# Kernel tuning notes

Measured on AMD Instinct MI355X. Metric: run time of the kernel, lower is better.

Reference implementation:

```python
import jax, jax.numpy as jnp
import numpy as np

N, E = 20000, 320000
H1, C1 = 8, 128   # gat1 heads/out
H2, C2 = 1, 128   # gat2 heads/out
D_IN = 768
NEG_SLOPE = 0.2
BN_EPS = 1e-5


def setup_inputs() -> dict:
    key = jax.random.key(0)
    ks = jax.random.split(key, 16)
    def rn(k, shape, fan):
        return jax.random.normal(k, shape, dtype=jnp.float32) / np.sqrt(fan)
    x = jax.random.normal(ks[0], (N, D_IN), dtype=jnp.float32)
    edge_index = jax.random.randint(ks[1], (2, E), 0, N, dtype=jnp.int64)
    return {
        "x": x,
        "edge_index": edge_index,
        "W1": rn(ks[2], (D_IN, H1 * C1), D_IN),
        "att_src1": rn(ks[3], (H1, C1), C1),
        "att_dst1": rn(ks[4], (H1, C1), C1),
        "b1": jnp.zeros((H1 * C1,), jnp.float32),
        "W2": rn(ks[5], (H1 * C1, H2 * C2), H1 * C1),
        "att_src2": rn(ks[6], (H2, C2), C2),
        "att_dst2": rn(ks[7], (H2, C2), C2),
        "b2": jnp.zeros((C2,), jnp.float32),
        "g1": jnp.ones((H1 * C1,), jnp.float32),
        "be1": jnp.zeros((H1 * C1,), jnp.float32),
        "g2": jnp.ones((C2,), jnp.float32),
        "be2": jnp.zeros((C2,), jnp.float32),
        "Wc1": rn(ks[8], (C2, 64), C2),
        "bc1": jnp.zeros((64,), jnp.float32),
        "Wc2": rn(ks[9], (64, 2), 64),
        "bc2": jnp.zeros((2,), jnp.float32),
    }


def gat_conv(x, src, dst, W, att_src, att_dst, bias, heads, ch, concat):
    n = x.shape[0]
    h = (x @ W).reshape(n, heads, ch)                      # [N,H,C]
    a_s = jnp.sum(h * att_src[None], axis=-1)              # [N,H]
    a_d = jnp.sum(h * att_dst[None], axis=-1)
    e = a_s[src] + a_d[dst]                                # [Et,H]
    e = jax.nn.leaky_relu(e, NEG_SLOPE)
    # segment softmax over incoming edges of each dst node
    m = jax.ops.segment_max(e, dst, num_segments=n)
    ex = jnp.exp(e - m[dst])
    z = jax.ops.segment_sum(ex, dst, num_segments=n)
    alpha = ex / z[dst]                                    # [Et,H]
    msg = alpha[:, :, None] * h[src]                       # [Et,H,C]
    out = jax.ops.segment_sum(msg, dst, num_segments=n)    # [N,H,C]
    if concat:
        out = out.reshape(n, heads * ch)
    else:
        out = out.mean(axis=1)
    return out + bias


def batch_norm(x, gamma, beta):
    mu = x.mean(axis=0)
    var = x.var(axis=0)
    return (x - mu) * jax.lax.rsqrt(var + BN_EPS) * gamma + beta


def reference(x, edge_index, W1, att_src1, att_dst1, b1, W2, att_src2, att_dst2, b2,
              g1, be1, g2, be2, Wc1, bc1, Wc2, bc2):
    n = x.shape[0]
    loop = jnp.arange(n, dtype=edge_index.dtype)
    src = jnp.concatenate([edge_index[0], loop])  # PyG add_self_loops default
    dst = jnp.concatenate([edge_index[1], loop])
    h = gat_conv(x, src, dst, W1, att_src1, att_dst1, b1, H1, C1, True)
    h = jax.nn.elu(batch_norm(h, g1, be1))
    h = gat_conv(h, src, dst, W2, att_src2, att_dst2, b2, H2, C2, False)
    h = jax.nn.elu(batch_norm(h, g2, be2))
    h = jax.nn.relu(h @ Wc1 + bc1)
    return h @ Wc2 + bc2
```

## Files before the change

kernel.cpp:

```cpp
#include <hip/hip_runtime.h>
#include <hip/hip_bf16.h>
#include <math.h>

#define N_NODES 20000
#define N_EDGES 320000
#define DIN 768
#define F1 1024
#define H1 8
#define C1 128
#define F2 128
#define NEG_SLOPE 0.2f
#define BN_EPS 1e-5f
#define RESCALE_THR 8.0f

typedef __attribute__((ext_vector_type(8))) __bf16 bf16x8;
typedef __attribute__((ext_vector_type(4))) float f32x4;

__device__ __forceinline__ float leaky(float x) { return x > 0.f ? x : NEG_SLOPE * x; }

__device__ __forceinline__ unsigned short f2bu(float x) {
  __hip_bfloat16 b = __float2bfloat16(x);
  return *(unsigned short*)&b;
}
__device__ __forceinline__ float b2f(unsigned short u) {
  return __uint_as_float(((unsigned)u) << 16);
}
__device__ __forceinline__ unsigned pack2(float lo, float hi) {
  return (unsigned)f2bu(lo) | ((unsigned)f2bu(hi) << 16);
}

__device__ __forceinline__ void async_copy16(void* lds, const void* g) {
  __builtin_amdgcn_global_load_lds(
      (const __attribute__((address_space(1))) unsigned int*)g,
      (__attribute__((address_space(3))) unsigned int*)lds, 16, 0, 0);
}

__global__ void repack_hist_kernel(const int* raw, int* ei32, int* deg) {
  int is64 = (raw[1] == 0 && raw[3] == 0 && raw[5] == 0 && raw[7] == 0) ? 1 : 0;
  int e = blockIdx.x * blockDim.x + threadIdx.x;
  if (e < 2 * N_EDGES) {
    int v = is64 ? raw[2 * e] : raw[e];
    ei32[e] = v;
    if (e >= N_EDGES) atomicAdd(&deg[v], 1);
  }
}

#define NPT 20
__global__ __launch_bounds__(1024) void scan_kernel(const int* __restrict__ deg,
                                                    int* __restrict__ off,
                                                    int* __restrict__ cursor) {
  __shared__ int wsum[16];
  int tid = threadIdx.x;
  int lane = tid & 63, wv = tid >> 6;
  int base = tid * NPT;
  int loc[NPT];
  int run = 0;
#pragma unroll
  for (int k = 0; k < NPT; ++k) {
    int i = base + k;
    int v = (i < N_NODES) ? deg[i] : 0;
    loc[k] = run;
    run += v;
  }
  int incl = run;
  for (int sh = 1; sh < 64; sh <<= 1) {
    int t = __shfl_up(incl, sh, 64);
    if (lane >= sh) incl += t;
  }
  if (lane == 63) wsum[wv] = incl;
  __syncthreads();
  if (wv == 0 && lane < 16) {
    int v = wsum[lane];
    for (int sh = 1; sh < 16; sh <<= 1) {
      int t = __shfl_up(v, sh, 16);
      if (lane >= sh) v += t;
    }
    wsum[lane] = v;
  }
  __syncthreads();
  int wbase = (wv > 0) ? wsum[wv - 1] : 0;
  int tbase = wbase + incl - run;
#pragma unroll
  for (int k = 0; k < NPT; ++k) {
    int i = base + k;
    if (i < N_NODES) {
      int o = tbase + loc[k];
      off[i] = o;
      cursor[i] = o;
    }
  }
  if (tid == 1023) off[N_NODES] = wbase + incl;
}

__global__ void scatter_kernel(const int* ei, int* cursor, int* elist) {
  int e = blockIdx.x * blockDim.x + threadIdx.x;
  if (e < N_EDGES) {
    int dst = ei[N_EDGES + e];
    int p = atomicAdd(&cursor[dst], 1);
    elist[p] = ei[e];
  }
}

__global__ void f2b_kernel(const float* __restrict__ in, unsigned short* __restrict__ out,
                           size_t n4) {
  size_t i = (size_t)blockIdx.x * blockDim.x + threadIdx.x;
  size_t stride = (size_t)gridDim.x * blockDim.x;
  for (; i < n4; i += stride) {
    float4 v = ((const float4*)in)[i];
    ushort4 u;
    u.x = f2bu(v.x); u.y = f2bu(v.y); u.z = f2bu(v.z); u.w = f2bu(v.w);
    ((ushort4*)out)[i] = u;
  }
}

__global__ void transpose_b_kernel(const float* __restrict__ W, unsigned short* __restrict__ WT,
                                   int K, int N) {
  __shared__ float t[32][33];
  int k0 = blockIdx.y * 32, n0 = blockIdx.x * 32;
  int tx = threadIdx.x & 31, ty = threadIdx.x >> 5;
  for (int i = 0; i < 32; i += 8)
    t[ty + i][tx] = W[(size_t)(k0 + ty + i) * N + n0 + tx];
  __syncthreads();
  for (int i = 0; i < 32; i += 8)
    WT[(size_t)(n0 + ty + i) * K + k0 + tx] = f2bu(t[tx][ty + i]);
}

#define GBM 128
#define GBN 128
#define GBK 64
template <int H, int SWZ>
__global__ __launch_bounds__(256) void mfma_gemm_att_kernel(
    const unsigned short* __restrict__ A,
    const unsigned short* __restrict__ BT,
    unsigned short* __restrict__ C,
    const float* __restrict__ att_src,
    const float* __restrict__ att_dst,
    float* __restrict__ as_out,
    float* __restrict__ ad_out,
    int M, int N, int K) {
  __shared__ __hip_bfloat16 As[GBM][GBK];
  __shared__ __hip_bfloat16 Bs[GBN][GBK];
  __shared__ float sred[128][2];
  __shared__ float dred[128][2];
  int bx, by;
  if (SWZ) {
    int bid = blockIdx.x;
    int pl = bid & 7, c = (bid >> 3) & 7, ph = bid >> 6;
    int p = ph * 8 + pl;
    if (p * GBM >= M) return;
    by = p; bx = c;
  } else {
    bx = blockIdx.x; by = blockIdx.y;
  }
  int tid = threadIdx.x;
  int lane = tid & 63, wid = tid >> 6;
  int wr = wid >> 1, wc = wid & 1;
  int row0 = by * GBM, col0 = bx * GBN;
  int head = bx;
  int l16 = lane & 15, l4 = lane >> 4;
  f32x4 acc[4][4] = {};
  for (int k0 = 0; k0 < K; k0 += GBK) {
#pragma unroll
    for (int j = 0; j < 4; ++j) {
      int c = j * 256 + tid;
      int r = c >> 3, kk = (c & 7) << 3;
      int ga = row0 + r; if (ga >= M) ga = M - 1;
      async_copy16(&As[r][kk], A + (size_t)ga * K + k0 + kk);
      async_copy16(&Bs[r][kk], BT + (size_t)(col0 + r) * K + k0 + kk);
    }
    __syncthreads();
#pragma unroll
    for (int ks = 0; ks < 2; ++ks) {
      bf16x8 af[4], bfr[4];
#pragma unroll
      for (int i = 0; i < 4; ++i)
        af[i] = *(const bf16x8*)&As[wr * 64 + i * 16 + l16][ks * 32 + l4 * 8];
#pragma unroll
      for (int j = 0; j < 4; ++j)
        bfr[j] = *(const bf16x8*)&Bs[wc * 64 + j * 16 + l16][ks * 32 + l4 * 8];
#pragma unroll
      for (int i = 0; i < 4; ++i)
#pragma unroll
        for (int j = 0; j < 4; ++j)
          acc[i][j] = __builtin_amdgcn_mfma_f32_16x16x32_bf16(af[i], bfr[j], acc[i][j], 0, 0, 0);
    }
    __syncthreads();
  }
#pragma unroll
  for (int i = 0; i < 4; ++i) {
#pragma unroll
    for (int j = 0; j < 4; ++j) {
#pragma unroll
      for (int r = 0; r < 4; ++r) {
        int row = row0 + wr * 64 + i * 16 + l4 * 4 + r;
        int col = col0 + wc * 64 + j * 16 + l16;
        if (row < M) C[(size_t)row * N + col] = f2bu(acc[i][j][r]);
      }
    }
  }
  float avs[4], avd[4];
#pragma unroll
  for (int j = 0; j < 4; ++j) {
    int col = col0 + wc * 64 + j * 16 + l16;
    avs[j] = att_src[col];
    avd[j] = att_dst[col];
  }
#pragma unroll
  for (int i = 0; i < 4; ++i) {
#pragma unroll
    for (int r = 0; r < 4; ++r) {
      float ps = 0.f, pd = 0.f;
#pragma unroll
      for (int j = 0; j < 4; ++j) { ps += acc[i][j][r] * avs[j]; pd += acc[i][j][r] * avd[j]; }
#pragma unroll
      for (int mk = 1; mk < 16; mk <<= 1) {
        ps += __shfl_xor(ps, mk, 64);
        pd += __shfl_xor(pd, mk, 64);
      }
      if (l16 == 0) {
        int lr = wr * 64 + i * 16 + l4 * 4 + r;
        sred[lr][wc] = ps;
        dred[lr][wc] = pd;
      }
    }
  }
  __syncthreads();
  if (tid < 128) {
    int row = row0 + tid;
    if (row < M) {
      as_out[(size_t)row * H + head] = sred[tid][0] + sred[tid][1];
      ad_out[(size_t)row * H + head] = dred[tid][0] + dred[tid][1];
    }
  }
}

__global__ __launch_bounds__(64) void alpha1_kernel(const float* __restrict__ as1,
                                                    const float* __restrict__ ad1,
                                                    const int* __restrict__ off,
                                                    const int* __restrict__ elist,
                                                    float* __restrict__ wexpT,
                                                    float* __restrict__ zinv,
                                                    float* __restrict__ wself) {
  int node = blockIdx.x;
  int lane = threadIdx.x;
  int s = off[node], e = off[node + 1];
#pragma unroll
  for (int h = 0; h < H1; ++h) {
    float ad = ad1[node * H1 + h];
    float selfl = leaky(as1[node * H1 + h] + ad);
    float m = selfl;
    for (int i = s + lane; i < e; i += 64) {
      float el = leaky(as1[elist[i] * H1 + h] + ad);
      m = fmaxf(m, el);
    }
    for (int sh = 32; sh >= 1; sh >>= 1) m = fmaxf(m, __shfl_xor(m, sh, 64));
    float z = 0.f;
    for (int i = s + lane; i < e; i += 64) {
      float el = leaky(as1[elist[i] * H1 + h] + ad);
      float w = __expf(el - m);
      wexpT[(size_t)h * N_EDGES + i] = w;
      z += w;
    }
    for (int sh = 32; sh >= 1; sh >>= 1) z += __shfl_xor(z, sh, 64);
    float ws = __expf(selfl - m);
    if (lane == 0) {
      zinv[node * H1 + h] = 1.f / (z + ws);
      wself[node * H1 + h] = ws;
    }
  }
}

#define GW_LOAD(i, rv, wv)                                                     \
  if ((i) < e) {                                                               \
    wv = wp[(i)];                                                              \
    rv = *(const unsigned*)(h1 + (size_t)elist[(i)] * F1 + cb);                \
  }
#define GW_CONS(u, wv)                                                         \
  {                                                                            \
    a0 += wv * __uint_as_float(u << 16);                                       \
    a1 += wv * __uint_as_float(u & 0xffff0000u);                               \
  }

__global__ __launch_bounds__(64) void gatherw1_kernel(const unsigned short* __restrict__ h1,
                                                      const float* __restrict__ wexpT,
                                                      const float* __restrict__ zinv,
                                                      const float* __restrict__ wself,
                                                      const int* __restrict__ off,
                                                      const int* __restrict__ elist,
                                                      const float* __restrict__ b1,
                                                      unsigned short* __restrict__ out1) {
  int head = blockIdx.x;
  int node = blockIdx.y;
  int tid = threadIdx.x;
  int cb = head * C1 + tid * 2;
  int s = off[node], e = off[node + 1];
  const float* wp = wexpT + (size_t)head * N_EDGES;
  float a0, a1;
  {
    float ws = wself[node * H1 + head];
    unsigned u = *(const unsigned*)(h1 + (size_t)node * F1 + cb);
    a0 = ws * __uint_as_float(u << 16);
    a1 = ws * __uint_as_float(u & 0xffff0000u);
  }
  unsigned ra0 = 0, ra1 = 0, ra2 = 0, ra3 = 0;
  float wa0 = 0.f, wa1 = 0.f, wa2 = 0.f, wa3 = 0.f;
  GW_LOAD(s + 0, ra0, wa0)
  GW_LOAD(s + 1, ra1, wa1)
  GW_LOAD(s + 2, ra2, wa2)
  GW_LOAD(s + 3, ra3, wa3)
  for (int base = s; base < e; base += 4) {
    unsigned rb0 = 0, rb1 = 0, rb2 = 0, rb3 = 0;
    float wb0 = 0.f, wb1 = 0.f, wb2 = 0.f, wb3 = 0.f;
    int nb = base + 4;
    GW_LOAD(nb + 0, rb0, wb0)
    GW_LOAD(nb + 1, rb1, wb1)
    GW_LOAD(nb + 2, rb2, wb2)
    GW_LOAD(nb + 3, rb3, wb3)
    GW_CONS(ra0, wa0)
    GW_CONS(ra1, wa1)
    GW_CONS(ra2, wa2)
    GW_CONS(ra3, wa3)
    ra0 = rb0; ra1 = rb1; ra2 = rb2; ra3 = rb3;
    wa0 = wb0; wa1 = wb1; wa2 = wb2; wa3 = wb3;
  }
  float inv = zinv[node * H1 + head];
  float2 bv = *(const float2*)(b1 + cb);
  unsigned o = pack2(a0 * inv + bv.x, a1 * inv + bv.y);
  *(unsigned*)(out1 + (size_t)node * F1 + cb) = o;
}

__global__ void bnstats_bf16_kernel(const unsigned short* __restrict__ x,
                                    float* __restrict__ sums,
                                    int nrows, int F, int rowsPerBlock) {
  int tid = threadIdx.x;
  int c = tid * 4;
  int r0 = blockIdx.x * rowsPerBlock;
  int rend = min(r0 + rowsPerBlock, nrows);
  float s0 = 0.f, s1 = 0.f, s2 = 0.f, s3 = 0.f;
  float q0 = 0.f, q1 = 0.f, q2 = 0.f, q3 = 0.f;
  for (int r = r0; r < rend; ++r) {
    ushort4 u = *(const ushort4*)(x + (size_t)r * F + c);
    float v0 = b2f(u.x), v1 = b2f(u.y), v2 = b2f(u.z), v3 = b2f(u.w);
    s0 += v0; s1 += v1; s2 += v2; s3 += v3;
    q0 += v0 * v0; q1 += v1 * v1; q2 += v2 * v2; q3 += v3 * v3;
  }
  atomicAdd(&sums[c + 0], s0); atomicAdd(&sums[c + 1], s1);
  atomicAdd(&sums[c + 2], s2); atomicAdd(&sums[c + 3], s3);
  atomicAdd(&sums[F + c + 0], q0); atomicAdd(&sums[F + c + 1], q1);
  atomicAdd(&sums[F + c + 2], q2); atomicAdd(&sums[F + c + 3], q3);
}

template <int CPT>
__global__ void bnstats_kernel(const float* __restrict__ x, float* __restrict__ sums,
                               int nrows, int F, int rowsPerBlock) {
  int tid = threadIdx.x;
  int r0 = blockIdx.x * rowsPerBlock;
  int rend = min(r0 + rowsPerBlock, nrows);
  float s[CPT], q[CPT];
#pragma unroll
  for (int k = 0; k < CPT; ++k) { s[k] = 0.f; q[k] = 0.f; }
  for (int r = r0; r < rend; ++r) {
    const float* row = x + (size_t)r * F;
#pragma unroll
    for (int k = 0; k < CPT; ++k) {
      float v = row[tid + k * blockDim.x];
      s[k] += v; q[k] += v * v;
    }
  }
#pragma unroll
  for (int k = 0; k < CPT; ++k) {
    atomicAdd(&sums[tid + k * blockDim.x], s[k]);
    atomicAdd(&sums[F + tid + k * blockDim.x], q[k]);
  }
}

__global__ void bnfinal_kernel(const float* __restrict__ sums, const float* __restrict__ g,
                               const float* __restrict__ be, float* __restrict__ ss, int F) {
  int c = blockIdx.x * blockDim.x + threadIdx.x;
  if (c < F) {
    float mu = sums[c] * (1.f / N_NODES);
    float var = sums[F + c] * (1.f / N_NODES) - mu * mu;
    float sc = g[c] * rsqrtf(var + BN_EPS);
    ss[c] = sc;
    ss[F + c] = be[c] - mu * sc;
  }
}

__global__ void bnapply_bf16_kernel(unsigned short* __restrict__ x, const float* __restrict__ ss,
                                    int F, size_t total4) {
  size_t i = (size_t)blockIdx.x * blockDim.x + threadIdx.x;
  size_t stride = (size_t)gridDim.x * blockDim.x;
  for (; i < total4; i += stride) {
    int c = (int)((i * 4) & (size_t)(F - 1));
    ushort4 u = ((ushort4*)x)[i];
    float v0 = b2f(u.x) * ss[c + 0] + ss[F + c + 0];
    float v1 = b2f(u.y) * ss[c + 1] + ss[F + c + 1];
    float v2 = b2f(u.z) * ss[c + 2] + ss[F + c + 2];
    float v3 = b2f(u.w) * ss[c + 3] + ss[F + c + 3];
    v0 = v0 > 0.f ? v0 : expm1f(v0);
    v1 = v1 > 0.f ? v1 : expm1f(v1);
    v2 = v2 > 0.f ? v2 : expm1f(v2);
    v3 = v3 > 0.f ? v3 : expm1f(v3);
    u.x = f2bu(v0); u.y = f2bu(v1); u.z = f2bu(v2); u.w = f2bu(v3);
    ((ushort4*)x)[i] = u;
  }
}

#define G2_LOAD(i, rv, ev)                                                     \
  if ((i) < e) {                                                               \
    int ssrc = elist[(i)];                                                     \
    ev = leaky(as2[ssrc] + ad);                                                \
    rv = *(const unsigned*)(h2 + (size_t)ssrc * F2 + tid * 2);                 \
  }
#define G2_CONSUME(u, el)                                                      \
  {                                                                            \
    float w;                                                                   \
    if (el > m + RESCALE_THR) {                                                \
      float rr = __expf(m - el);                                               \
      z *= rr; a0 *= rr; a1 *= rr;                                             \
      m = el; w = 1.f;                                                         \
    } else {                                                                   \
      w = __expf(el - m);                                                      \
    }                                                                          \
    z += w;                                                                    \
    a0 += w * __uint_as_float(u << 16);                                        \
    a1 += w * __uint_as_float(u & 0xffff0000u);                                \
  }

__global__ __launch_bounds__(64) void gather2_kernel(const unsigned short* __restrict__ h2,
                                                     const float* __restrict__ as2,
                                                     const float* __restrict__ ad2,
                                                     const int* __restrict__ off,
                                                     const int* __restrict__ elist,
                                                     const float* __restrict__ b2,
                                                     float* __restrict__ out2) {
  int node = blockIdx.x;
  int tid = threadIdx.x;
  const float ad = ad2[node];
  int s = off[node], e = off[node + 1];
  float m = leaky(as2[node] + ad);
  float z = 1.f;
  float a0, a1;
  {
    unsigned u = *(const unsigned*)(h2 + (size_t)node * F2 + tid * 2);
    a0 = __uint_as_float(u << 16); a1 = __uint_as_float(u & 0xffff0000u);
  }
  unsigned ra0 = 0, ra1 = 0, ra2 = 0, ra3 = 0;
  float ea0 = 0.f, ea1 = 0.f, ea2 = 0.f, ea3 = 0.f;
  G2_LOAD(s + 0, ra0, ea0)
  G2_LOAD(s + 1, ra1, ea1)
  G2_LOAD(s + 2, ra2, ea2)
  G2_LOAD(s + 3, ra3, ea3)
  for (int base = s; base < e; base += 4) {
    unsigned rb0 = 0, rb1 = 0, rb2 = 0, rb3 = 0;
    float eb0 = 0.f, eb1 = 0.f, eb2 = 0.f, eb3 = 0.f;
    int nb = base + 4;
    G2_LOAD(nb + 0, rb0, eb0)
    G2_LOAD(nb + 1, rb1, eb1)
    G2_LOAD(nb + 2, rb2, eb2)
    G2_LOAD(nb + 3, rb3, eb3)
    G2_CONSUME(ra0, ea0)
    if (base + 1 < e) G2_CONSUME(ra1, ea1)
    if (base + 2 < e) G2_CONSUME(ra2, ea2)
    if (base + 3 < e) G2_CONSUME(ra3, ea3)
    ra0 = rb0; ra1 = rb1; ra2 = rb2; ra3 = rb3;
    ea0 = eb0; ea1 = eb1; ea2 = eb2; ea3 = eb3;
  }
  float inv = 1.f / z;
  float2 o = make_float2(a0 * inv + b2[tid * 2 + 0], a1 * inv + b2[tid * 2 + 1]);
  *(float2*)(out2 + (size_t)node * F2 + tid * 2) = o;
}

__global__ __launch_bounds__(64) void cls_kernel(const float* __restrict__ h,
                                                 const float* __restrict__ ss2,
                                                 const float* __restrict__ Wc1,
                                                 const float* __restrict__ bc1,
                                                 const float* __restrict__ Wc2,
                                                 const float* __restrict__ bc2,
                                                 float* __restrict__ out) {
  __shared__ float hl[128];
  int node = blockIdx.x;
  int tid = threadIdx.x;
  {
    float v = h[(size_t)node * F2 + tid] * ss2[tid] + ss2[F2 + tid];
    v = v > 0.f ? v : expm1f(v);
    hl[tid] = v;
    float v2 = h[(size_t)node * F2 + 64 + tid] * ss2[64 + tid] + ss2[F2 + 64 + tid];
    v2 = v2 > 0.f ? v2 : expm1f(v2);
    hl[tid + 64] = v2;
  }
  __syncthreads();
  float acc = bc1[tid];
#pragma unroll
  for (int k = 0; k < 128; ++k) acc += hl[k] * Wc1[k * 64 + tid];
  acc = fmaxf(acc, 0.f);
  float2 w = *(const float2*)(Wc2 + tid * 2);
  float o0 = acc * w.x, o1 = acc * w.y;
  for (int sh = 32; sh >= 1; sh >>= 1) {
    o0 += __shfl_down(o0, sh, 64);
    o1 += __shfl_down(o1, sh, 64);
  }
  if (tid == 0) {
    out[node * 2 + 0] = o0 + bc2[0];
    out[node * 2 + 1] = o1 + bc2[1];
  }
}

extern "C" void kernel_launch(void* const* d_in, const int* in_sizes, int n_in,
                              void* d_out, int out_size, void* d_ws, size_t ws_size,
                              hipStream_t stream) {
  const float* x        = (const float*)d_in[0];
  const int*   ei_raw   = (const int*)d_in[1];
  const float* W1       = (const float*)d_in[2];
  const float* att_src1 = (const float*)d_in[3];
  const float* att_dst1 = (const float*)d_in[4];
  const float* b1       = (const float*)d_in[5];
  const float* W2       = (const float*)d_in[6];
  const float* att_src2 = (const float*)d_in[7];
  const float* att_dst2 = (const float*)d_in[8];
  const float* b2       = (const float*)d_in[9];
  const float* g1       = (const float*)d_in[10];
  const float* be1      = (const float*)d_in[11];
  const float* g2       = (const float*)d_in[12];
  const float* be2      = (const float*)d_in[13];
  const float* Wc1      = (const float*)d_in[14];
  const float* bc1      = (const float*)d_in[15];
  const float* Wc2      = (const float*)d_in[16];
  const float* bc2      = (const float*)d_in[17];
  float* out = (float*)d_out;

  char* ws = (char*)d_ws;
  size_t o = 0;
  unsigned short* h1b   = (unsigned short*)(ws + o); o += (size_t)N_NODES * F1 * 2;
  unsigned short* out1b = (unsigned short*)(ws + o); o += (size_t)N_NODES * F1 * 2;
  unsigned short* xb    = (unsigned short*)(ws + o); o += (size_t)N_NODES * DIN * 2;
  unsigned short* h2b   = (unsigned short*)(ws + o); o += (size_t)N_NODES * F2 * 2;
  float* out2  = (float*)(ws + o); o += (size_t)N_NODES * F2 * 4;
  float* as1   = (float*)(ws + o); o += (size_t)N_NODES * H1 * 4;
  float* ad1   = (float*)(ws + o); o += (size_t)N_NODES * H1 * 4;
  float* as2   = (float*)(ws + o); o += (size_t)N_NODES * 4;
  float* ad2   = (float*)(ws + o); o += (size_t)N_NODES * 4;
  float* wexpT = (float*)(ws + o); o += (size_t)H1 * N_EDGES * 4;
  float* zinv  = (float*)(ws + o); o += (size_t)N_NODES * H1 * 4;
  float* wself = (float*)(ws + o); o += (size_t)N_NODES * H1 * 4;
  char*  zbase = ws + o;
  float* bnsum1 = (float*)(ws + o); o += F1 * 2 * 4;
  float* bnsum2 = (float*)(ws + o); o += F2 * 2 * 4;
  int*   deg    = (int*)(ws + o); o += (size_t)N_NODES * 4;
  size_t zbytes = (size_t)((ws + o) - zbase);
  int*   offv   = (int*)(ws + o); o += (size_t)(N_NODES + 4) * 4;
  int*   cursor = (int*)(ws + o); o += (size_t)N_NODES * 4;
  int*   elist  = (int*)(ws + o); o += (size_t)N_EDGES * 4;
  float* ss1    = (float*)(ws + o); o += F1 * 2 * 4;
  float* ss2    = (float*)(ws + o); o += F2 * 2 * 4;
  int*   ei32   = (int*)(ws + o); o += (size_t)2 * N_EDGES * 4;
  unsigned short* W1T = (unsigned short*)(ws + o); o += (size_t)F1 * DIN * 2;
  unsigned short* W2T = (unsigned short*)(ws + o); o += (size_t)F2 * F1 * 2;
  (void)ws_size; (void)in_sizes; (void)n_in; (void)out_size;

  hipMemsetAsync((void*)zbase, 0, zbytes, stream);

  f2b_kernel<<<2048, 256, 0, stream>>>(x, xb, (size_t)N_NODES * DIN / 4);
  {
    dim3 g1d(F1 / 32, DIN / 32);
    transpose_b_kernel<<<g1d, 256, 0, stream>>>(W1, W1T, DIN, F1);
    dim3 g2d(F2 / 32, F1 / 32);
    transpose_b_kernel<<<g2d, 256, 0, stream>>>(W2, W2T, F1, F2);
  }

  repack_hist_kernel<<<(2 * N_EDGES + 255) / 256, 256, 0, stream>>>(ei_raw, ei32, deg);
  scan_kernel<<<1, 1024, 0, stream>>>(deg, offv, cursor);
  scatter_kernel<<<(N_EDGES + 255) / 256, 256, 0, stream>>>(ei32, cursor, elist);

  {
    int panels = (N_NODES + GBM - 1) / GBM;
    int grid1 = ((panels + 7) / 8) * 64;
    mfma_gemm_att_kernel<H1, 1><<<grid1, 256, 0, stream>>>(
        xb, W1T, h1b, att_src1, att_dst1, as1, ad1, N_NODES, F1, DIN);
  }
  alpha1_kernel<<<N_NODES, 64, 0, stream>>>(as1, ad1, offv, elist, wexpT, zinv, wself);
  gatherw1_kernel<<<dim3(H1, N_NODES), 64, 0, stream>>>(
      h1b, wexpT, zinv, wself, offv, elist, b1, out1b);
  {
    int rows = 79;
    int grid = (N_NODES + rows - 1) / rows;
    bnstats_bf16_kernel<<<grid, 256, 0, stream>>>(out1b, bnsum1, N_NODES, F1, rows);
  }
  bnfinal_kernel<<<(F1 + 255) / 256, 256, 0, stream>>>(bnsum1, g1, be1, ss1, F1);
  bnapply_bf16_kernel<<<2048, 256, 0, stream>>>(out1b, ss1, F1, (size_t)N_NODES * F1 / 4);

  {
    dim3 grid(F2 / GBN, (N_NODES + GBM - 1) / GBM);
    mfma_gemm_att_kernel<1, 0><<<grid, 256, 0, stream>>>(
        out1b, W2T, h2b, att_src2, att_dst2, as2, ad2, N_NODES, F2, F1);
  }
  gather2_kernel<<<N_NODES, 64, 0, stream>>>(h2b, as2, ad2, offv, elist, b2, out2);
  {
    int rows = 79;
    int grid = (N_NODES + rows - 1) / rows;
    bnstats_kernel<1><<<grid, 128, 0, stream>>>(out2, bnsum2, N_NODES, F2, rows);
  }
  bnfinal_kernel<<<1, F2, 0, stream>>>(bnsum2, g2, be2, ss2, F2);

  cls_kernel<<<N_NODES, 64, 0, stream>>>(out2, ss2, Wc1, bc1, Wc2, bc2, out);
}
```

Before: 461.7 us.

## Pack source index with edge weight and deepen gather prefetch pipeline

alpha1 now handles all 8 heads in one pass per edge, loading each source's 8 attention scores as two float4s instead of re-walking the edge list once per head. It writes (src, weight) pairs per head, so the gather kernel no longer does a dependent elist lookup before fetching h1 rows. The gather loop now prefetches edge pairs two stages ahead, which shortens the chain of dependent loads. In exchange the edge-weight buffer doubles in size, so alpha1 writes more bytes and the gather reads more, and register use rises.

```diff
diff --git a/kernel.cpp b/kernel.cpp
--- a/kernel.cpp
+++ b/kernel.cpp
@@ -238,55 +238,74 @@
                                                     const float* __restrict__ ad1,
                                                     const int* __restrict__ off,
                                                     const int* __restrict__ elist,
-                                                    float* __restrict__ wexpT,
+                                                    uint2* __restrict__ ewT,
                                                     float* __restrict__ zinv,
                                                     float* __restrict__ wself) {
   int node = blockIdx.x;
   int lane = threadIdx.x;
   int s = off[node], e = off[node + 1];
-#pragma unroll
-  for (int h = 0; h < H1; ++h) {
-    float ad = ad1[node * H1 + h];
-    float selfl = leaky(as1[node * H1 + h] + ad);
-    float m = selfl;
-    for (int i = s + lane; i < e; i += 64) {
-      float el = leaky(as1[elist[i] * H1 + h] + ad);
-      m = fmaxf(m, el);
-    }
-    for (int sh = 32; sh >= 1; sh >>= 1) m = fmaxf(m, __shfl_xor(m, sh, 64));
-    float z = 0.f;
-    for (int i = s + lane; i < e; i += 64) {
-      float el = leaky(as1[elist[i] * H1 + h] + ad);
-      float w = __expf(el - m);
-      wexpT[(size_t)h * N_EDGES + i] = w;
-      z += w;
-    }
-    for (int sh = 32; sh >= 1; sh >>= 1) z += __shfl_xor(z, sh, 64);
-    float ws = __expf(selfl - m);
-    if (lane == 0) {
-      zinv[node * H1 + h] = 1.f / (z + ws);
+  float4 adlo = *(const float4*)(ad1 + node * H1);
+  float4 adhi = *(const float4*)(ad1 + node * H1 + 4);
+  float ad[8] = {adlo.x, adlo.y, adlo.z, adlo.w, adhi.x, adhi.y, adhi.z, adhi.w};
+  float4 aslo = *(const float4*)(as1 + node * H1);
+  float4 ashi = *(const float4*)(as1 + node * H1 + 4);
+  float sl[8] = {aslo.x, aslo.y, aslo.z, aslo.w, ashi.x, ashi.y, ashi.z, ashi.w};
+  float m[8];
+#pragma unroll
+  for (int h = 0; h < 8; ++h) { sl[h] = leaky(sl[h] + ad[h]); m[h] = sl[h]; }
+  for (int i = s + lane; i < e; i += 64) {
+    int src = elist[i];
+    float4 lo = *(const float4*)(as1 + (size_t)src * H1);
+    float4 hi = *(const float4*)(as1 + (size_t)src * H1 + 4);
+    float v[8] = {lo.x, lo.y, lo.z, lo.w, hi.x, hi.y, hi.z, hi.w};
+#pragma unroll
+    for (int h = 0; h < 8; ++h) m[h] = fmaxf(m[h], leaky(v[h] + ad[h]));
+  }
+#pragma unroll
+  for (int h = 0; h < 8; ++h)
+    for (int sh = 32; sh >= 1; sh >>= 1) m[h] = fmaxf(m[h], __shfl_xor(m[h], sh, 64));
+  float z[8] = {0.f, 0.f, 0.f, 0.f, 0.f, 0.f, 0.f, 0.f};
+  for (int i = s + lane; i < e; i += 64) {
+    int src = elist[i];
+    float4 lo = *(const float4*)(as1 + (size_t)src * H1);
+    float4 hi = *(const float4*)(as1 + (size_t)src * H1 + 4);
+    float v[8] = {lo.x, lo.y, lo.z, lo.w, hi.x, hi.y, hi.z, hi.w};
+#pragma unroll
+    for (int h = 0; h < 8; ++h) {
+      float w = __expf(leaky(v[h] + ad[h]) - m[h]);
+      z[h] += w;
+      ewT[(size_t)h * N_EDGES + i] = make_uint2((unsigned)src, __float_as_uint(w));
+    }
+  }
+#pragma unroll
+  for (int h = 0; h < 8; ++h)
+    for (int sh = 32; sh >= 1; sh >>= 1) z[h] += __shfl_xor(z[h], sh, 64);
+  if (lane == 0) {
+#pragma unroll
+    for (int h = 0; h < 8; ++h) {
+      float ws = __expf(sl[h] - m[h]);
+      zinv[node * H1 + h] = 1.f / (z[h] + ws);
       wself[node * H1 + h] = ws;
     }
   }
 }
 
-#define GW_LOAD(i, rv, wv)                                                     \
-  if ((i) < e) {                                                               \
-    wv = wp[(i)];                                                              \
-    rv = *(const unsigned*)(h1 + (size_t)elist[(i)] * F1 + cb);                \
-  }
-#define GW_CONS(u, wv)                                                         \
-  {                                                                            \
-    a0 += wv * __uint_as_float(u << 16);                                       \
-    a1 += wv * __uint_as_float(u & 0xffff0000u);                               \
+#define EW_LOAD(i, ev)                                                          \
+  if ((i) < e) ev = ewp[(i)];
+#define H1_LOAD(i, ev, rv)                                                      \
+  if ((i) < e) rv = *(const unsigned*)(h1 + (size_t)ev.x * F1 + cb);
+#define GW_CONS(u, ev)                                                          \
+  {                                                                             \
+    float wv = __uint_as_float(ev.y);                                           \
+    a0 += wv * __uint_as_float(u << 16);                                        \
+    a1 += wv * __uint_as_float(u & 0xffff0000u);                                \
   }
 
 __global__ __launch_bounds__(64) void gatherw1_kernel(const unsigned short* __restrict__ h1,
-                                                      const float* __restrict__ wexpT,
+                                                      const uint2* __restrict__ ewT,
                                                       const float* __restrict__ zinv,
                                                       const float* __restrict__ wself,
                                                       const int* __restrict__ off,
-                                                      const int* __restrict__ elist,
                                                       const float* __restrict__ b1,
                                                       unsigned short* __restrict__ out1) {
   int head = blockIdx.x;
@@ -294,7 +313,7 @@
   int tid = threadIdx.x;
   int cb = head * C1 + tid * 2;
   int s = off[node], e = off[node + 1];
-  const float* wp = wexpT + (size_t)head * N_EDGES;
+  const uint2* ewp = ewT + (size_t)head * N_EDGES;
   float a0, a1;
   {
     float ws = wself[node * H1 + head];
@@ -302,26 +321,41 @@
     a0 = ws * __uint_as_float(u << 16);
     a1 = ws * __uint_as_float(u & 0xffff0000u);
   }
+  uint2 ea0 = {0, 0}, ea1 = {0, 0}, ea2 = {0, 0}, ea3 = {0, 0};
+  uint2 eb0 = {0, 0}, eb1 = {0, 0}, eb2 = {0, 0}, eb3 = {0, 0};
   unsigned ra0 = 0, ra1 = 0, ra2 = 0, ra3 = 0;
-  float wa0 = 0.f, wa1 = 0.f, wa2 = 0.f, wa3 = 0.f;
-  GW_LOAD(s + 0, ra0, wa0)
-  GW_LOAD(s + 1, ra1, wa1)
-  GW_LOAD(s + 2, ra2, wa2)
-  GW_LOAD(s + 3, ra3, wa3)
+  EW_LOAD(s + 0, ea0)
+  EW_LOAD(s + 1, ea1)
+  EW_LOAD(s + 2, ea2)
+  EW_LOAD(s + 3, ea3)
+  EW_LOAD(s + 4, eb0)
+  EW_LOAD(s + 5, eb1)
+  EW_LOAD(s + 6, eb2)
+  EW_LOAD(s + 7, eb3)
+  H1_LOAD(s + 0, ea0, ra0)
+  H1_LOAD(s + 1, ea1, ra1)
+  H1_LOAD(s + 2, ea2, ra2)
+  H1_LOAD(s + 3, ea3, ra3)
   for (int base = s; base < e; base += 4) {
     unsigned rb0 = 0, rb1 = 0, rb2 = 0, rb3 = 0;
-    float wb0 = 0.f, wb1 = 0.f, wb2 = 0.f, wb3 = 0.f;
     int nb = base + 4;
-    GW_LOAD(nb + 0, rb0, wb0)
-    GW_LOAD(nb + 1, rb1, wb1)
-    GW_LOAD(nb + 2, rb2, wb2)
-    GW_LOAD(nb + 3, rb3, wb3)
-    GW_CONS(ra0, wa0)
-    GW_CONS(ra1, wa1)
-    GW_CONS(ra2, wa2)
-    GW_CONS(ra3, wa3)
+    H1_LOAD(nb + 0, eb0, rb0)
+    H1_LOAD(nb + 1, eb1, rb1)
+    H1_LOAD(nb + 2, eb2, rb2)
+    H1_LOAD(nb + 3, eb3, rb3)
+    uint2 ec0 = {0, 0}, ec1 = {0, 0}, ec2 = {0, 0}, ec3 = {0, 0};
+    int nc = base + 8;
+    EW_LOAD(nc + 0, ec0)
+    EW_LOAD(nc + 1, ec1)
+    EW_LOAD(nc + 2, ec2)
+    EW_LOAD(nc + 3, ec3)
+    GW_CONS(ra0, ea0)
+    GW_CONS(ra1, ea1)
+    GW_CONS(ra2, ea2)
+    GW_CONS(ra3, ea3)
+    ea0 = eb0; ea1 = eb1; ea2 = eb2; ea3 = eb3;
+    eb0 = ec0; eb1 = ec1; eb2 = ec2; eb3 = ec3;
     ra0 = rb0; ra1 = rb1; ra2 = rb2; ra3 = rb3;
-    wa0 = wb0; wa1 = wb1; wa2 = wb2; wa3 = wb3;
   }
   float inv = zinv[node * H1 + head];
   float2 bv = *(const float2*)(b1 + cb);
@@ -540,7 +574,7 @@
   float* ad1   = (float*)(ws + o); o += (size_t)N_NODES * H1 * 4;
   float* as2   = (float*)(ws + o); o += (size_t)N_NODES * 4;
   float* ad2   = (float*)(ws + o); o += (size_t)N_NODES * 4;
-  float* wexpT = (float*)(ws + o); o += (size_t)H1 * N_EDGES * 4;
+  uint2* ewT   = (uint2*)(ws + o); o += (size_t)H1 * N_EDGES * 8;
   float* zinv  = (float*)(ws + o); o += (size_t)N_NODES * H1 * 4;
   float* wself = (float*)(ws + o); o += (size_t)N_NODES * H1 * 4;
   char*  zbase = ws + o;
@@ -578,9 +612,9 @@
     mfma_gemm_att_kernel<H1, 1><<<grid1, 256, 0, stream>>>(
         xb, W1T, h1b, att_src1, att_dst1, as1, ad1, N_NODES, F1, DIN);
   }
-  alpha1_kernel<<<N_NODES, 64, 0, stream>>>(as1, ad1, offv, elist, wexpT, zinv, wself);
+  alpha1_kernel<<<N_NODES, 64, 0, stream>>>(as1, ad1, offv, elist, ewT, zinv, wself);
   gatherw1_kernel<<<dim3(H1, N_NODES), 64, 0, stream>>>(
-      h1b, wexpT, zinv, wself, offv, elist, b1, out1b);
+      h1b, ewT, zinv, wself, offv, b1, out1b);
   {
     int rows = 79;
     int grid = (N_NODES + rows - 1) / rows;
```

New measurement: 447.6 us. 3.0% less time.
